# Kernel optimization log

Measured on AMD Instinct MI355X. Metric: run time of the kernel, lower is better.

## Reference

```python
import jax, jax.numpy as jnp
import numpy as np

B, QLEN, KLEN = 4, 512, 1024
KDIM = QDIM = ADIM = 512
H_MA, H_CA = 4, 2
CHUNK = 4
EPS = 1e-6
SHARP = 1.0
SCALE = float(np.sqrt(ADIM))


def moving_sum(x, back, forward):
    # moving sum over last axis with window [i-back, i+forward] (matches F.conv1d with ones filter)
    nb = [(0, 0)] * (x.ndim - 1)
    cs = jnp.cumsum(jnp.pad(x, nb + [(back, forward)]), axis=-1)
    cs = jnp.pad(cs, nb + [(1, 0)])
    w = back + forward + 1
    return cs[..., w:] - cs[..., :-w]


def setup_inputs() -> dict:
    key = jax.random.key(0)
    ks = jax.random.split(key, 16)
    s = 0.02
    f32 = jnp.float32
    return {
        'key_t': jax.random.normal(ks[0], (B, KLEN, KDIM), f32),
        'query': jax.random.normal(ks[1], (B, QLEN, QDIM), f32),
        # monotonic energy params
        'wk_ma': jax.random.normal(ks[2], (KDIM, ADIM), f32) * s,
        'bk_ma': jnp.zeros((ADIM,), f32),
        'wq_ma': jax.random.normal(ks[3], (QDIM, ADIM), f32) * s,
        'bq_ma': jnp.zeros((ADIM,), f32),
        'r': jnp.array([-4.0], f32),
        # chunk energy params
        'wk_ca': jax.random.normal(ks[4], (KDIM, ADIM), f32) * s,
        'bk_ca': jnp.zeros((ADIM,), f32),
        'wq_ca': jax.random.normal(ks[5], (QDIM, ADIM), f32) * s,
        'bq_ca': jnp.zeros((ADIM,), f32),
        # value / output projections
        'wv': jax.random.normal(ks[6], (KDIM, ADIM), f32) * s,
        'bv': jnp.zeros((ADIM,), f32),
        'wo': jax.random.normal(ks[7], (ADIM, ADIM), f32) * s,
        'bo': jnp.zeros((ADIM,), f32),
    }


def reference(key_t, query, wk_ma, bk_ma, wq_ma, bq_ma, r,
              wk_ca, bk_ca, wq_ca, bq_ca, wv, bv, wo, bo):
    # ---- monotonic energy (scaled_dot) -> [B, H_ma, qlen, klen]
    dk = ADIM // H_MA
    k_ma = (key_t @ wk_ma + bk_ma).reshape(B, KLEN, H_MA, dk).transpose(0, 2, 1, 3)
    q_ma = (query @ wq_ma + bq_ma).reshape(B, QLEN, H_MA, dk).transpose(0, 2, 1, 3)
    e_ma = jnp.einsum('bhqd,bhkd->bhqk', q_ma, k_ma) / SCALE + r[0]

    # ---- selection probabilities + safe cumprod of (1 - p) (exclusive, in log space)
    p = jax.nn.sigmoid(e_ma)                              # [B,H,q,k]
    log1mp = jnp.log(jnp.clip(1.0 - p, EPS, 1.0))
    cp = jnp.exp(jnp.cumsum(log1mp, axis=-1) - log1mp)    # exclusive cumprod

    # ---- monotonic alignment alpha via recurrence over query steps (parallel MoChA)
    aw0 = jnp.zeros((B, H_MA, KLEN), p.dtype).at[:, :, 0].set(1.0)

    def step(aw_prev, pc):
        p_i, cp_i = pc  # [B,H,k]
        a = p_i * cp_i * jnp.cumsum(aw_prev / jnp.clip(cp_i, EPS, 1.0), axis=-1)
        return a, a

    _, alpha_q = jax.lax.scan(step, aw0, (jnp.moveaxis(p, 2, 0), jnp.moveaxis(cp, 2, 0)))
    alpha = jnp.moveaxis(alpha_q, 0, 2)                   # [B,H_ma,q,k]

    # ---- chunk energy (scaled_dot, shared across MA heads) -> [B, H_ca, qlen, klen]
    dkc = ADIM // H_CA
    k_ca = (key_t @ wk_ca + bk_ca).reshape(B, KLEN, H_CA, dkc).transpose(0, 2, 1, 3)
    q_ca = (query @ wq_ca + bq_ca).reshape(B, QLEN, H_CA, dkc).transpose(0, 2, 1, 3)
    e_ca = jnp.einsum('bhqd,bhkd->bhqk', q_ca, k_ca) / SCALE

    # ---- efficient chunkwise attention: clipped-exp softmax within moving window
    u = e_ca - jnp.max(e_ca, axis=-1, keepdims=True)
    se = jnp.maximum(jnp.exp(u), 1e-5)                    # [B,H_ca,q,k]
    denom = moving_sum(se, CHUNK - 1, 0)                  # [B,H_ca,q,k]
    frac = alpha[:, :, None] * SHARP / denom[:, None]     # [B,H_ma,H_ca,q,k]
    beta = se[:, None] * moving_sum(frac, 0, CHUNK - 1)   # [B,H_ma,H_ca,q,k]
    beta = beta.reshape(B, H_MA * H_CA, QLEN, KLEN)

    # ---- context vector and output projection
    h = H_MA * H_CA
    dv = ADIM // h
    v = (key_t @ wv + bv).reshape(B, KLEN, h, dv).transpose(0, 2, 1, 3)
    cv = jnp.einsum('bhqk,bhkd->bhqd', beta, v)
    cv = cv.transpose(0, 2, 1, 3).reshape(B, QLEN, ADIM)
    return cv @ wo + bo
```

## Files before the change

### kernel.cpp

```cpp
#include <hip/hip_runtime.h>
#include <hip/hip_bf16.h>
#include <math.h>

#define DEV_INLINE __device__ __forceinline__

typedef float f32x4 __attribute__((ext_vector_type(4)));
typedef short bf16x8 __attribute__((ext_vector_type(8)));
typedef short s16x4 __attribute__((ext_vector_type(4)));

constexpr int B_    = 4;
constexpr int QLEN  = 512;
constexpr int KLEN  = 1024;
constexpr int DIM   = 512;
constexpr int H_MA  = 4;
constexpr int H_CA  = 2;
constexpr int CHUNK = 4;
constexpr float EPS = 1e-6f;
constexpr float INV_SCALE = 1.0f / 22.62741699796952f;


DEV_INLINE unsigned short f2bf(float x) {
    unsigned int u = __float_as_uint(x);
    unsigned int r = u + 0x7FFFu + ((u >> 16) & 1u);
    return (unsigned short)(r >> 16);
}

DEV_INLINE void split2(float x, short& h, short& l) {
    const unsigned short hb = f2bf(x);
    const float hf = __uint_as_float(((unsigned int)hb) << 16);
    h = (short)hb;
    l = (short)f2bf(x - hf);
}

DEV_INLINE float bf2f(short s) {
    return __uint_as_float(((unsigned int)(unsigned short)s) << 16);
}

__global__ __launch_bounds__(256) void rowsplit2_kernel(
    const float* __restrict__ X0, short* __restrict__ H0, short* __restrict__ L0, int n0_4,
    const float* __restrict__ X1, short* __restrict__ H1, short* __restrict__ L1, int n1_4)
{
    int i = blockIdx.x * 256 + threadIdx.x;
    const float* X; short* Xh; short* Xl;
    if (i < n0_4) { X = X0; Xh = H0; Xl = L0; }
    else {
        i -= n0_4;
        if (i >= n1_4) return;
        X = X1; Xh = H1; Xl = L1;
    }
    const f32x4 v = *(const f32x4*)(X + (size_t)i * 4);
    s16x4 h, l;
#pragma unroll
    for (int j = 0; j < 4; ++j) {
        short hh, ll;
        split2(v[j], hh, ll);
        h[j] = hh; l[j] = ll;
    }
    *(s16x4*)(Xh + (size_t)i * 4) = h;
    *(s16x4*)(Xl + (size_t)i * 4) = l;
}

__global__ __launch_bounds__(256) void transsplit6_kernel(
    const float* __restrict__ w0, const float* __restrict__ w1,
    const float* __restrict__ w2, const float* __restrict__ w3,
    const float* __restrict__ w4, const float* __restrict__ w5,
    short* __restrict__ WTkh, short* __restrict__ WTkl,
    short* __restrict__ WTqh, short* __restrict__ WTql,
    short* __restrict__ WToh, short* __restrict__ WTol)
{
    const float* W; short* Dh; short* Dl;
    const int zz = blockIdx.z;
    const int MS = 512 * 512;
    switch (zz) {
        case 0: W = w0; Dh = WTkh;          Dl = WTkl;          break;
        case 1: W = w1; Dh = WTkh + MS;     Dl = WTkl + MS;     break;
        case 2: W = w2; Dh = WTkh + 2 * MS; Dl = WTkl + 2 * MS; break;
        case 3: W = w3; Dh = WTqh;          Dl = WTql;          break;
        case 4: W = w4; Dh = WTqh + MS;     Dl = WTql + MS;     break;
        default: W = w5; Dh = WToh;         Dl = WTol;          break;
    }

    __shared__ __align__(16) short Th[64][72];
    __shared__ __align__(16) short Tl[64][72];
    const int t = threadIdx.x;
    const int k0 = blockIdx.x * 64;
    const int n0 = blockIdx.y * 64;
#pragma unroll
    for (int i = 0; i < 4; ++i) {
        const int c  = t + 256 * i;
        const int kr = c >> 4;
        const int nc = c & 15;
        const f32x4 v = *(const f32x4*)(W + (size_t)(k0 + kr) * DIM + n0 + nc * 4);
#pragma unroll
        for (int j = 0; j < 4; ++j) {
            short h, l;
            split2(v[j], h, l);
            Th[nc * 4 + j][kr] = h;
            Tl[nc * 4 + j][kr] = l;
        }
    }
    __syncthreads();
#pragma unroll
    for (int i = 0; i < 4; ++i) {
        const int c  = t + 256 * i;
        const int nr = c >> 4;
        const int kc = c & 15;
        *(s16x4*)(Dh + (size_t)(n0 + nr) * DIM + k0 + kc * 4) = *(const s16x4*)&Th[nr][kc * 4];
        *(s16x4*)(Dl + (size_t)(n0 + nr) * DIM + k0 + kc * 4) = *(const s16x4*)&Tl[nr][kc * 4];
    }
}


DEV_INLINE void mfma128_nt_core(
    const short* __restrict__ Ah, const short* __restrict__ Al, int lda,
    const short* __restrict__ Bh, const short* __restrict__ Bl, int ldb,
    int K, int bm, int bn, f32x4 (&acc)[4][4])
{
    __shared__ __align__(16) short AsH[8][4][16][8];
    __shared__ __align__(16) short AsL[8][4][16][8];
    __shared__ __align__(16) short BsH[8][4][16][8];
    __shared__ __align__(16) short BsL[8][4][16][8];
    const int tid  = threadIdx.x;
    const int lane = tid & 63;
    const int w    = tid >> 6;
    const int wm   = w >> 1, wn = w & 1;
    const int lkg  = lane >> 4, lrow = lane & 15;

    for (int k0 = 0; k0 < K; k0 += 32) {
        bf16x8 vah[2], val[2], vbh[2], vbl[2];
#pragma unroll
        for (int p = 0; p < 2; ++p) {
            const int c = p * 256 + tid;
            const int row = c >> 2, kk = c & 3;
            const size_t ao = (size_t)(bm + row) * lda + k0 + kk * 8;
            const size_t bo = (size_t)(bn + row) * ldb + k0 + kk * 8;
            vah[p] = *(const bf16x8*)(Ah + ao);
            val[p] = *(const bf16x8*)(Al + ao);
            vbh[p] = *(const bf16x8*)(Bh + bo);
            vbl[p] = *(const bf16x8*)(Bl + bo);
        }
        __syncthreads();
#pragma unroll
        for (int p = 0; p < 2; ++p) {
            const int c = p * 256 + tid;
            const int row = c >> 2, kk = c & 3;
            const int fm = row >> 4, rr = row & 15;
            *(bf16x8*)&AsH[fm][kk][rr][0] = vah[p];
            *(bf16x8*)&AsL[fm][kk][rr][0] = val[p];
            *(bf16x8*)&BsH[fm][kk][rr][0] = vbh[p];
            *(bf16x8*)&BsL[fm][kk][rr][0] = vbl[p];
        }
        __syncthreads();

        bf16x8 bhf[4], blf[4];
#pragma unroll
        for (int fn = 0; fn < 4; ++fn) {
            bhf[fn] = *(const bf16x8*)&BsH[wn * 4 + fn][lkg][lrow][0];
            blf[fn] = *(const bf16x8*)&BsL[wn * 4 + fn][lkg][lrow][0];
        }
#pragma unroll
        for (int fm = 0; fm < 4; ++fm) {
            const bf16x8 ah = *(const bf16x8*)&AsH[wm * 4 + fm][lkg][lrow][0];
            const bf16x8 al = *(const bf16x8*)&AsL[wm * 4 + fm][lkg][lrow][0];
#pragma unroll
            for (int fn = 0; fn < 4; ++fn) {
                acc[fm][fn] = __builtin_amdgcn_mfma_f32_16x16x32_bf16(ah, bhf[fn], acc[fm][fn], 0, 0, 0);
                acc[fm][fn] = __builtin_amdgcn_mfma_f32_16x16x32_bf16(ah, blf[fn], acc[fm][fn], 0, 0, 0);
                acc[fm][fn] = __builtin_amdgcn_mfma_f32_16x16x32_bf16(al, bhf[fn], acc[fm][fn], 0, 0, 0);
            }
        }
    }
}

__global__ __launch_bounds__(256) void proj_both_kernel(
    const short* __restrict__ Kh, const short* __restrict__ Kl,
    const short* __restrict__ Qh, const short* __restrict__ Ql,
    const short* __restrict__ WTkh, const short* __restrict__ WTkl,
    const short* __restrict__ WTqh, const short* __restrict__ WTql,
    short* __restrict__ KPh, short* __restrict__ KPl,
    short* __restrict__ QPh, short* __restrict__ QPl,
    const float* __restrict__ bkma, const float* __restrict__ bkca,
    const float* __restrict__ bvv_,
    const float* __restrict__ bqma, const float* __restrict__ bqca)
{
    const int bid = blockIdx.x;
    const short *Ah, *Al, *Bh, *Bl;
    short *Ch, *Cl;
    const float *b0, *b1, *b2;
    int bm, bn, ldc;
    if (bid < 384) {
        bm = (bid & 31) * 128; bn = (bid >> 5) * 128;
        Ah = Kh; Al = Kl; Bh = WTkh; Bl = WTkl;
        Ch = KPh; Cl = KPl; ldc = 1536;
        b0 = bkma; b1 = bkca; b2 = bvv_;
    } else {
        const int r = bid - 384;
        bm = (r & 15) * 128; bn = (r >> 4) * 128;
        Ah = Qh; Al = Ql; Bh = WTqh; Bl = WTql;
        Ch = QPh; Cl = QPl; ldc = 1024;
        b0 = bqma; b1 = bqca; b2 = bqca;
    }

    f32x4 acc[4][4] = {};
    mfma128_nt_core(Ah, Al, DIM, Bh, Bl, DIM, DIM, bm, bn, acc);
    const int lane = threadIdx.x & 63;
    const int w = threadIdx.x >> 6;
    const int wm = w >> 1, wn = w & 1;
#pragma unroll
    for (int fm = 0; fm < 4; ++fm)
#pragma unroll
        for (int fn = 0; fn < 4; ++fn) {
            const int col = bn + wn * 64 + fn * 16 + (lane & 15);
            const int seg = col >> 9, cs = col & 511;
            const float bvv = seg == 0 ? b0[cs] : (seg == 1 ? b1[cs] : b2[cs]);
#pragma unroll
            for (int j = 0; j < 4; ++j) {
                const int row = bm + wm * 64 + fm * 16 + (lane >> 4) * 4 + j;
                short h, l;
                split2(acc[fm][fn][j] + bvv, h, l);
                Ch[(size_t)row * ldc + col] = h;
                Cl[(size_t)row * ldc + col] = l;
            }
        }
}

__global__ __launch_bounds__(256) void energy_both_kernel(
    const short* __restrict__ QPh, const short* __restrict__ QPl,
    const short* __restrict__ KPh, const short* __restrict__ KPl,
    float* __restrict__ EMA, float* __restrict__ ECA,
    const float* __restrict__ radd)
{
    const int gz = blockIdx.z;
    int colA0, colB0, HD;
    float* E;
    float addv;
    int b, h;
    if (gz < 16) {
        b = gz >> 2; h = gz & 3;
        colA0 = 0; colB0 = 0; HD = 128;
        E = EMA + (size_t)gz * QLEN * KLEN;
        addv = radd[0];
    } else {
        const int z = gz - 16;
        b = z >> 1; h = z & 1;
        colA0 = 512; colB0 = 512; HD = 256;
        E = ECA + (size_t)z * QLEN * KLEN;
        addv = 0.0f;
    }
    const short* Ah = QPh + (size_t)b * QLEN * 1024 + colA0 + h * HD;
    const short* Al = QPl + (size_t)b * QLEN * 1024 + colA0 + h * HD;
    const short* Bh = KPh + (size_t)b * KLEN * 1536 + colB0 + h * HD;
    const short* Bl = KPl + (size_t)b * KLEN * 1536 + colB0 + h * HD;

    f32x4 acc[4][4] = {};
    const int bm = blockIdx.x * 128, bn = blockIdx.y * 128;
    mfma128_nt_core(Ah, Al, 1024, Bh, Bl, 1536, HD, bm, bn, acc);
    const int lane = threadIdx.x & 63;
    const int w = threadIdx.x >> 6;
    const int wm = w >> 1, wn = w & 1;
#pragma unroll
    for (int fm = 0; fm < 4; ++fm)
#pragma unroll
        for (int fn = 0; fn < 4; ++fn) {
            const int col = bn + wn * 64 + fn * 16 + (lane & 15);
#pragma unroll
            for (int j = 0; j < 4; ++j) {
                const int row = bm + wm * 64 + fm * 16 + (lane >> 4) * 4 + j;
                E[(size_t)row * KLEN + col] = acc[fm][fn][j] * INV_SCALE + addv;
            }
        }
}


DEV_INLINE void mfma_nt_core(const short* __restrict__ Ah, const short* __restrict__ Al, int lda,
                             const short* __restrict__ Bh, const short* __restrict__ Bl, int ldb,
                             int K, int bm, int bn, f32x4 (&acc)[2][2])
{
    __shared__ __align__(16) short AsH[4][4][16][8];
    __shared__ __align__(16) short AsL[4][4][16][8];
    __shared__ __align__(16) short BsH[4][4][16][8];
    __shared__ __align__(16) short BsL[4][4][16][8];
    const int tid  = threadIdx.x;
    const int lane = tid & 63;
    const int w    = tid >> 6;
    const int wm   = w >> 1, wn = w & 1;
    const int r    = tid >> 2;
    const int kg   = tid & 3;
    const int rb   = r >> 4, rr = r & 15;
    const int lkg  = lane >> 4, lrr = lane & 15;

    for (int k0 = 0; k0 < K; k0 += 32) {
        const bf16x8 avh = *(const bf16x8*)(Ah + (size_t)(bm + r) * lda + k0 + kg * 8);
        const bf16x8 avl = *(const bf16x8*)(Al + (size_t)(bm + r) * lda + k0 + kg * 8);
        const bf16x8 bvh = *(const bf16x8*)(Bh + (size_t)(bn + r) * ldb + k0 + kg * 8);
        const bf16x8 bvl = *(const bf16x8*)(Bl + (size_t)(bn + r) * ldb + k0 + kg * 8);
        __syncthreads();
        *(bf16x8*)&AsH[rb][kg][rr][0] = avh;
        *(bf16x8*)&AsL[rb][kg][rr][0] = avl;
        *(bf16x8*)&BsH[rb][kg][rr][0] = bvh;
        *(bf16x8*)&BsL[rb][kg][rr][0] = bvl;
        __syncthreads();
#pragma unroll
        for (int fm = 0; fm < 2; ++fm) {
            const bf16x8 ah = *(const bf16x8*)&AsH[wm * 2 + fm][lkg][lrr][0];
            const bf16x8 al = *(const bf16x8*)&AsL[wm * 2 + fm][lkg][lrr][0];
#pragma unroll
            for (int fn = 0; fn < 2; ++fn) {
                const bf16x8 bh = *(const bf16x8*)&BsH[wn * 2 + fn][lkg][lrr][0];
                const bf16x8 bl = *(const bf16x8*)&BsL[wn * 2 + fn][lkg][lrr][0];
                acc[fm][fn] = __builtin_amdgcn_mfma_f32_16x16x32_bf16(ah, bh, acc[fm][fn], 0, 0, 0);
                acc[fm][fn] = __builtin_amdgcn_mfma_f32_16x16x32_bf16(ah, bl, acc[fm][fn], 0, 0, 0);
                acc[fm][fn] = __builtin_amdgcn_mfma_f32_16x16x32_bf16(al, bh, acc[fm][fn], 0, 0, 0);
            }
        }
    }
}

__global__ __launch_bounds__(256) void mfma_nt_f32_kernel(
    const short* __restrict__ Ah, const short* __restrict__ Al, int lda,
    const short* __restrict__ Bh, const short* __restrict__ Bl, int ldb,
    float* __restrict__ C, int ldc, int K,
    const float* __restrict__ bias)
{
    f32x4 acc[2][2] = {};
    const int bm = blockIdx.x * 64, bn = blockIdx.y * 64;
    mfma_nt_core(Ah, Al, lda, Bh, Bl, ldb, K, bm, bn, acc);
    const int lane = threadIdx.x & 63;
    const int w = threadIdx.x >> 6;
    const int wm = w >> 1, wn = w & 1;
#pragma unroll
    for (int fm = 0; fm < 2; ++fm)
#pragma unroll
        for (int fn = 0; fn < 2; ++fn) {
            const int col = bn + wn * 32 + fn * 16 + (lane & 15);
            const float bvv = bias ? bias[col] : 0.0f;
#pragma unroll
            for (int j = 0; j < 4; ++j) {
                const int row = bm + wm * 32 + fm * 16 + (lane >> 4) * 4 + j;
                C[(size_t)row * ldc + col] = acc[fm][fn][j] + bvv;
            }
        }
}


__global__ __launch_bounds__(256) void rows_kernel(
    float* __restrict__ PCP, float* __restrict__ ICP,
    float* __restrict__ SE, float* __restrict__ RDEN)
{
    const int bid = blockIdx.x;
    const int tid = threadIdx.x;
    const int lane = tid & 63, wid = tid >> 6;

    if (bid < B_ * H_MA * QLEN) {
        const size_t row = bid;
        float* pe = PCP + row * KLEN;
        float* pi = ICP + row * KLEN;

        const float4 ev = *(const float4*)(pe + tid * 4);
        float e[4] = {ev.x, ev.y, ev.z, ev.w};
        float p[4], l[4], s[4];
        float run = 0.0f;
#pragma unroll
        for (int j = 0; j < 4; ++j) {
            p[j] = 1.0f / (1.0f + expf(-e[j]));
            float om = 1.0f - p[j];
            om = fminf(fmaxf(om, EPS), 1.0f);
            l[j] = logf(om);
            run += l[j];
            s[j] = run;
        }
        const float t = run;
        float v = t;
#pragma unroll
        for (int off = 1; off < 64; off <<= 1) {
            const float u = __shfl_up(v, off);
            if (lane >= off) v += u;
        }
        __shared__ float wsum[4];
        if (lane == 63) wsum[wid] = v;
        __syncthreads();
        float base = v - t;
        for (int w = 0; w < wid; ++w) base += wsum[w];

        float4 po, io;
        float* pp = (float*)&po;
        float* ip = (float*)&io;
#pragma unroll
        for (int j = 0; j < 4; ++j) {
            const float cum = base + s[j];
            const float cp  = expf(cum - l[j]);
            pp[j] = p[j] * cp;
            ip[j] = 1.0f / fmaxf(cp, EPS);
        }
        *(float4*)(pe + tid * 4) = po;
        *(float4*)(pi + tid * 4) = io;
    } else {
        const size_t row = bid - B_ * H_MA * QLEN;
        float* ps = SE + row * KLEN;
        float* pd = RDEN + row * KLEN;

        const float4 ev = *(const float4*)(ps + tid * 4);
        float e[4] = {ev.x, ev.y, ev.z, ev.w};
        float m = fmaxf(fmaxf(e[0], e[1]), fmaxf(e[2], e[3]));
#pragma unroll
        for (int off = 32; off >= 1; off >>= 1)
            m = fmaxf(m, __shfl_xor(m, off));
        __shared__ float wmax[4];
        if (lane == 0) wmax[wid] = m;
        __syncthreads();
        m = fmaxf(fmaxf(wmax[0], wmax[1]), fmaxf(wmax[2], wmax[3]));

        __shared__ float sh[KLEN + 3];
        if (tid < 3) sh[tid] = 0.0f;
        float se[4];
#pragma unroll
        for (int j = 0; j < 4; ++j) {
            se[j] = fmaxf(expf(e[j] - m), 1e-5f);
            sh[3 + tid * 4 + j] = se[j];
        }
        __syncthreads();
        float4 so, do_;
        float* sp = (float*)&so;
        float* dp = (float*)&do_;
#pragma unroll
        for (int j = 0; j < 4; ++j) {
            const int k = tid * 4 + j;
            sp[j] = se[j];
            dp[j] = 1.0f / (sh[3 + k] + sh[2 + k] + sh[1 + k] + sh[k]);
        }
        *(float4*)(ps + tid * 4) = so;
        *(float4*)(pd + tid * 4) = do_;
    }
}


template<int CTRL, int ROW_MASK>
DEV_INLINE float dpp_add(float x) {
    int t = __builtin_amdgcn_update_dpp(0, __float_as_int(x), CTRL, ROW_MASK, 0xf, true);
    return x + __int_as_float(t);
}

DEV_INLINE float wave64_incl_scan(float x) {
    x = dpp_add<0x111, 0xf>(x);
    x = dpp_add<0x112, 0xf>(x);
    x = dpp_add<0x114, 0xf>(x);
    x = dpp_add<0x118, 0xf>(x);
    x = dpp_add<0x142, 0xa>(x);
    x = dpp_add<0x143, 0xc>(x);
    return x;
}

typedef __attribute__((address_space(3))) void lv_t;
typedef __attribute__((address_space(1))) const void gv_t;

DEV_INLINE void dma16(const float* g, float* l) {
    __builtin_amdgcn_global_load_lds((gv_t*)g, (lv_t*)l, 16, 0, 0);
}

template<int N> DEV_INLINE void vwait() {
    asm volatile("s_waitcnt vmcnt(%0)" :: "i"(N) : "memory");
    __builtin_amdgcn_sched_barrier(0);
}

template<int N> DEV_INLINE void lwait() {
    asm volatile("s_waitcnt lgkmcnt(%0)" :: "i"(N));
    __builtin_amdgcn_sched_barrier(0);
}

DEV_INLINE void ldsr4(f32x4& d, const float* a_) {
    const unsigned off = (unsigned)(size_t)(lv_t*)a_;
    asm volatile("ds_read_b128 %0, %1" : "=v"(d) : "v"(off));
}

DEV_INLINE void dswr1(float* a_, float v) {
    const unsigned off = (unsigned)(size_t)(lv_t*)a_;
    asm volatile("ds_write_b32 %0, %1" :: "v"(off), "v"(v));
}

DEV_INLINE void sbar() {
    asm volatile("s_barrier" ::: "memory");
}

#define ASTEP(WAITN, BUF, NBUF, PAR, DO_READ, DO_DMA, CG, NG)         \
    {                                                                 \
        vwait<WAITN>();                                               \
        if (DO_READ) {                                                \
            ldsr4(p##NG, &ring[NBUF][0][qoff]);                       \
            ldsr4(i##NG, &ring[NBUF][1][qoff]);                       \
        }                                                             \
        const float t0 = a0 * i##CG[0];                               \
        const float t1 = a1 * i##CG[1];                               \
        const float t2 = a2 * i##CG[2];                               \
        const float t3 = a3 * i##CG[3];                               \
        const float s1 = t0 + t1;                                     \
        const float s2 = s1 + t2;                                     \
        const float s3 = s2 + t3;                                     \
        const float incl = wave64_incl_scan(s3);                      \
        const float excl = incl - s3;                                 \
        if (lane == 63) dswr1(&tot[PAR][wq], incl);                   \
        lwait<0>();                                                   \
        sbar();                                                       \
        f32x4 T;                                                      \
        ldsr4(T, &tot[PAR][0]);                                       \
        lwait<0>();                                                   \
        float Tpre = excl;                                            \
        if (wq > 0) Tpre += T[0];                                     \
        if (wq > 1) Tpre += T[1];                                     \
        if (wq > 2) Tpre += T[2];                                     \
        a0 = p##CG[0] * (Tpre + t0);                                  \
        a1 = p##CG[1] * (Tpre + s1);                                  \
        a2 = p##CG[2] * (Tpre + s2);                                  \
        a3 = p##CG[3] * (Tpre + s3);                                  \
        f32x4 av = {a0, a1, a2, a3};                                  \
        *(f32x4*)st = av;                                             \
        st += KLEN;                                                   \
        __builtin_amdgcn_sched_barrier(0);                            \
        if (DO_DMA) {                                                 \
            dma16(np, &ring[BUF][0][wq * 256]);                       \
            dma16(ni, &ring[BUF][1][wq * 256]);                       \
            np += KLEN; ni += KLEN;                                   \
        }                                                             \
    }

__global__ __launch_bounds__(256) void alpha_kernel(
    const float* __restrict__ PCPin, const float* __restrict__ ICP,
    float* __restrict__ AOUT)
{
    __shared__ __align__(16) float ring[8][2][1024];
    __shared__ __align__(16) float tot[2][4];

    const int z = blockIdx.x;
    const float* base = PCPin + (size_t)z * QLEN * KLEN;
    const float* ibase = ICP + (size_t)z * QLEN * KLEN;
    float* obase = AOUT + (size_t)z * QLEN * KLEN;
    const int tid  = threadIdx.x;
    const int lane = tid & 63;
    const int wq   = tid >> 6;
    const int qoff = wq * 256 + lane * 4;

    {
        const float* pp = base + qoff;
        const float* ip = ibase + qoff;
#pragma unroll
        for (int rr = 0; rr < 8; ++rr) {
            dma16(pp, &ring[rr][0][wq * 256]);
            dma16(ip, &ring[rr][1][wq * 256]);
            pp += KLEN; ip += KLEN;
        }
    }

    f32x4 pA, iA, pB, iB;
    vwait<14>();
    ldsr4(pA, &ring[0][0][qoff]);
    ldsr4(iA, &ring[0][1][qoff]);
    lwait<0>();

    float a0 = 0.0f, a1 = 0.0f, a2 = 0.0f, a3 = 0.0f;
    if (qoff == 0) a0 = 1.0f;

    float* st = obase + qoff;
    const float* np = base + (size_t)8 * KLEN + qoff;
    const float* ni = ibase + (size_t)8 * KLEN + qoff;

    for (int it = 0; it < 63; ++it) {
        ASTEP(12, 0, 1, 0, true, true, A, B)
        ASTEP(12, 1, 2, 1, true, true, B, A)
        ASTEP(12, 2, 3, 0, true, true, A, B)
        ASTEP(12, 3, 4, 1, true, true, B, A)
        ASTEP(12, 4, 5, 0, true, true, A, B)
        ASTEP(12, 5, 6, 1, true, true, B, A)
        ASTEP(12, 6, 7, 0, true, true, A, B)
        ASTEP(12, 7, 0, 1, true, true, B, A)
    }

    ASTEP(12, 0, 1, 0, true, false, A, B)
    ASTEP(10, 1, 2, 1, true, false, B, A)
    ASTEP(8,  2, 3, 0, true, false, A, B)
    ASTEP(6,  3, 4, 1, true, false, B, A)
    ASTEP(4,  4, 5, 0, true, false, A, B)
    ASTEP(2,  5, 6, 1, true, false, B, A)
    ASTEP(0,  6, 7, 0, true, false, A, B)
    ASTEP(0,  7, 0, 1, false, false, B, A)
}


__global__ __launch_bounds__(256) void fused_cv_kernel(
    const float* __restrict__ ALPHA, const float* __restrict__ SE,
    const float* __restrict__ RDEN,
    const short* __restrict__ VPh, const short* __restrict__ VPl, int ldv,
    short* __restrict__ CVh, short* __restrict__ CVl)
{
    const int z = blockIdx.y;
    const int b = z >> 3;
    const int h = z & 7;
    const int hma = h >> 1;
    const int hca = h & 1;
    const int bm = blockIdx.x * 64;

    const float* a_base  = ALPHA + ((size_t)b * H_MA + hma) * QLEN * KLEN;
    const float* se_base = SE   + ((size_t)b * H_CA + hca) * QLEN * KLEN;
    const float* dn_base = RDEN + ((size_t)b * H_CA + hca) * QLEN * KLEN;
    const short* vh_base = VPh + (size_t)b * KLEN * ldv + 1024 + h * 64;
    const short* vl_base = VPl + (size_t)b * KLEN * ldv + 1024 + h * 64;
    short* Ch = CVh + (size_t)b * QLEN * DIM + h * 64;
    short* Cl = CVl + (size_t)b * QLEN * DIM + h * 64;

    __shared__ float As[16][68];
    __shared__ float Bs[16][68];
    const int tid  = threadIdx.x;
    const int tm   = (tid >> 4) << 2;
    const int tn   = (tid & 15) << 2;
    const int arow = tid >> 2;
    const int acol = (tid & 3) << 2;
    const int brow = tid >> 4;
    const int bcol = (tid & 15) << 2;
    float acc[4][4] = {};

    for (int k0 = 0; k0 < KLEN; k0 += 16) {
        const int ka = k0 + acol;
        const size_t roff = (size_t)(bm + arow) * KLEN;
        const f32x4 sev = *(const f32x4*)(se_base + roff + ka);
        const f32x4 al0 = *(const f32x4*)(a_base + roff + ka);
        const f32x4 dn0 = *(const f32x4*)(dn_base + roff + ka);
        f32x4 al1 = {0.0f, 0.0f, 0.0f, 0.0f};
        f32x4 dn1 = {1.0f, 1.0f, 1.0f, 1.0f};
        if (ka + 4 < KLEN) {
            al1 = *(const f32x4*)(a_base + roff + ka + 4);
            dn1 = *(const f32x4*)(dn_base + roff + ka + 4);
        }
        float ad[7];
#pragma unroll
        for (int j = 0; j < 4; ++j) ad[j] = al0[j] * dn0[j];
#pragma unroll
        for (int j = 0; j < 3; ++j) ad[4 + j] = al1[j] * dn1[j];
        const s16x4 vh4 = *(const s16x4*)(vh_base + (size_t)(k0 + brow) * ldv + bcol);
        const s16x4 vl4 = *(const s16x4*)(vl_base + (size_t)(k0 + brow) * ldv + bcol);
        __syncthreads();
        As[acol + 0][arow] = sev[0] * (ad[0] + ad[1] + ad[2] + ad[3]);
        As[acol + 1][arow] = sev[1] * (ad[1] + ad[2] + ad[3] + ad[4]);
        As[acol + 2][arow] = sev[2] * (ad[2] + ad[3] + ad[4] + ad[5]);
        As[acol + 3][arow] = sev[3] * (ad[3] + ad[4] + ad[5] + ad[6]);
#pragma unroll
        for (int j = 0; j < 4; ++j)
            Bs[brow][bcol + j] = bf2f(vh4[j]) + bf2f(vl4[j]);
        __syncthreads();
#pragma unroll
        for (int kk = 0; kk < 16; ++kk) {
            const float4 av = *(const float4*)&As[kk][tm];
            const float4 bw = *(const float4*)&Bs[kk][tn];
            const float ar[4] = {av.x, av.y, av.z, av.w};
            const float br[4] = {bw.x, bw.y, bw.z, bw.w};
#pragma unroll
            for (int i = 0; i < 4; ++i)
#pragma unroll
                for (int j = 0; j < 4; ++j)
                    acc[i][j] = fmaf(ar[i], br[j], acc[i][j]);
        }
    }
#pragma unroll
    for (int i = 0; i < 4; ++i) {
        s16x4 oh, ol;
#pragma unroll
        for (int j = 0; j < 4; ++j) {
            short hh, ll;
            split2(acc[i][j], hh, ll);
            oh[j] = hh; ol[j] = ll;
        }
        const size_t ro = (size_t)(bm + tm + i) * DIM + tn;
        *(s16x4*)(Ch + ro) = oh;
        *(s16x4*)(Cl + ro) = ol;
    }
}


extern "C" void kernel_launch(void* const* d_in, const int* in_sizes, int n_in,
                              void* d_out, int out_size, void* d_ws, size_t ws_size,
                              hipStream_t stream)
{
    (void)in_sizes; (void)n_in; (void)out_size; (void)ws_size;
    const float* key_t = (const float*)d_in[0];
    const float* query = (const float*)d_in[1];
    const float* wk_ma = (const float*)d_in[2];
    const float* bk_ma = (const float*)d_in[3];
    const float* wq_ma = (const float*)d_in[4];
    const float* bq_ma = (const float*)d_in[5];
    const float* r     = (const float*)d_in[6];
    const float* wk_ca = (const float*)d_in[7];
    const float* bk_ca = (const float*)d_in[8];
    const float* wq_ca = (const float*)d_in[9];
    const float* bq_ca = (const float*)d_in[10];
    const float* wv    = (const float*)d_in[11];
    const float* bv    = (const float*)d_in[12];
    const float* wo    = (const float*)d_in[13];
    const float* bo    = (const float*)d_in[14];
    float* out = (float*)d_out;

    char* w8 = (char*)d_ws;
    size_t off = 0;
    auto take = [&](size_t n) { char* p = w8 + off; off += n; return p; };
    float* PCP = (float*)take(32ull << 20);
    float* ICP = (float*)take(32ull << 20);
    float* SE  = (float*)take(16ull << 20);
    float* DEN = (float*)take(16ull << 20);
    char* keyrg = take(8ull << 20);
    short* keyh = (short*)keyrg;
    short* keyl = (short*)(keyrg + (4ull << 20));
    short* CVh  = (short*)keyrg;
    short* CVl  = (short*)(keyrg + (2ull << 20));
    short* qh = (short*)take(2ull << 20);
    short* ql = (short*)take(2ull << 20);
    short* WTkh = (short*)take((size_t)1536 * 512 * 2);
    short* WTkl = (short*)take((size_t)1536 * 512 * 2);
    short* WTqh = (short*)take((size_t)1024 * 512 * 2);
    short* WTql = (short*)take((size_t)1024 * 512 * 2);
    short* WToh = (short*)take((size_t)512 * 512 * 2);
    short* WTol = (short*)take((size_t)512 * 512 * 2);
    short* KPh = (short*)take((size_t)4096 * 1536 * 2);
    short* KPl = (short*)take((size_t)4096 * 1536 * 2);
    short* QPh = (short*)take((size_t)2048 * 1024 * 2);
    short* QPl = (short*)take((size_t)2048 * 1024 * 2);

    const dim3 blk(256);
    const int KEL4 = B_ * KLEN * DIM / 4;
    const int QEL4 = B_ * QLEN * DIM / 4;

    rowsplit2_kernel<<<dim3((KEL4 + QEL4 + 255) / 256), blk, 0, stream>>>(
        key_t, keyh, keyl, KEL4, query, qh, ql, QEL4);
    transsplit6_kernel<<<dim3(8, 8, 6), blk, 0, stream>>>(
        wk_ma, wk_ca, wv, wq_ma, wq_ca, wo,
        WTkh, WTkl, WTqh, WTql, WToh, WTol);

    proj_both_kernel<<<dim3(512), blk, 0, stream>>>(
        keyh, keyl, qh, ql, WTkh, WTkl, WTqh, WTql,
        KPh, KPl, QPh, QPl, bk_ma, bk_ca, bv, bq_ma, bq_ca);

    energy_both_kernel<<<dim3(QLEN / 128, KLEN / 128, 24), blk, 0, stream>>>(
        QPh, QPl, KPh, KPl, PCP, SE, r);

    rows_kernel<<<dim3(B_ * H_MA * QLEN + B_ * H_CA * QLEN), blk, 0, stream>>>(
        PCP, ICP, SE, DEN);

    alpha_kernel<<<dim3(B_ * H_MA), blk, 0, stream>>>(PCP, ICP, PCP);

    fused_cv_kernel<<<dim3(QLEN / 64, B_ * H_MA * H_CA), blk, 0, stream>>>(
        PCP, SE, DEN, KPh, KPl, 1536, CVh, CVl);

    mfma_nt_f32_kernel<<<dim3(B_ * QLEN / 64, DIM / 64), blk, 0, stream>>>(
        CVh, CVl, DIM, WToh, WTol, DIM, out, DIM, DIM, bo);
}
```

Before: 328.6 us.

## Compute context vectors with split-bf16 MFMA instead of FP32 FMA loop

```diff
diff --git a/kernel.cpp b/kernel.cpp
--- a/kernel.cpp
+++ b/kernel.cpp
@@ -584,7 +584,7 @@
 }
 
 
-__global__ __launch_bounds__(256) void fused_cv_kernel(
+__global__ __launch_bounds__(256) void fused_cv_mfma_kernel(
     const float* __restrict__ ALPHA, const float* __restrict__ SE,
     const float* __restrict__ RDEN,
     const short* __restrict__ VPh, const short* __restrict__ VPl, int ldv,
@@ -605,71 +605,96 @@
     short* Ch = CVh + (size_t)b * QLEN * DIM + h * 64;
     short* Cl = CVl + (size_t)b * QLEN * DIM + h * 64;
 
-    __shared__ float As[16][68];
-    __shared__ float Bs[16][68];
+    __shared__ __align__(16) short AsH[4][4][16][8];
+    __shared__ __align__(16) short AsL[4][4][16][8];
+    __shared__ __align__(16) short BsH[4][4][16][8];
+    __shared__ __align__(16) short BsL[4][4][16][8];
+
     const int tid  = threadIdx.x;
-    const int tm   = (tid >> 4) << 2;
-    const int tn   = (tid & 15) << 2;
+    const int lane = tid & 63;
+    const int w    = tid >> 6;
+    const int wm   = w >> 1, wn = w & 1;
+    const int lkg  = lane >> 4, lrr = lane & 15;
     const int arow = tid >> 2;
-    const int acol = (tid & 3) << 2;
-    const int brow = tid >> 4;
-    const int bcol = (tid & 15) << 2;
-    float acc[4][4] = {};
-
-    for (int k0 = 0; k0 < KLEN; k0 += 16) {
-        const int ka = k0 + acol;
+    const int aoct = tid & 3;
+    const int vk  = tid >> 3;
+    const int vn8 = (tid & 7) * 8;
+
+    f32x4 acc[2][2] = {};
+
+    for (int k0 = 0; k0 < KLEN; k0 += 32) {
+        const int ka = k0 + aoct * 8;
         const size_t roff = (size_t)(bm + arow) * KLEN;
-        const f32x4 sev = *(const f32x4*)(se_base + roff + ka);
+        const f32x4 se0 = *(const f32x4*)(se_base + roff + ka);
+        const f32x4 se1 = *(const f32x4*)(se_base + roff + ka + 4);
         const f32x4 al0 = *(const f32x4*)(a_base + roff + ka);
+        const f32x4 al1 = *(const f32x4*)(a_base + roff + ka + 4);
         const f32x4 dn0 = *(const f32x4*)(dn_base + roff + ka);
-        f32x4 al1 = {0.0f, 0.0f, 0.0f, 0.0f};
-        f32x4 dn1 = {1.0f, 1.0f, 1.0f, 1.0f};
-        if (ka + 4 < KLEN) {
-            al1 = *(const f32x4*)(a_base + roff + ka + 4);
-            dn1 = *(const f32x4*)(dn_base + roff + ka + 4);
-        }
-        float ad[7];
+        const f32x4 dn1 = *(const f32x4*)(dn_base + roff + ka + 4);
+        f32x4 al2 = {0.0f, 0.0f, 0.0f, 0.0f};
+        f32x4 dn2 = {1.0f, 1.0f, 1.0f, 1.0f};
+        if (ka + 8 < KLEN) {
+            al2 = *(const f32x4*)(a_base + roff + ka + 8);
+            dn2 = *(const f32x4*)(dn_base + roff + ka + 8);
+        }
+        float ad[11];
 #pragma unroll
         for (int j = 0; j < 4; ++j) ad[j] = al0[j] * dn0[j];
 #pragma unroll
-        for (int j = 0; j < 3; ++j) ad[4 + j] = al1[j] * dn1[j];
-        const s16x4 vh4 = *(const s16x4*)(vh_base + (size_t)(k0 + brow) * ldv + bcol);
-        const s16x4 vl4 = *(const s16x4*)(vl_base + (size_t)(k0 + brow) * ldv + bcol);
-        __syncthreads();
-        As[acol + 0][arow] = sev[0] * (ad[0] + ad[1] + ad[2] + ad[3]);
-        As[acol + 1][arow] = sev[1] * (ad[1] + ad[2] + ad[3] + ad[4]);
-        As[acol + 2][arow] = sev[2] * (ad[2] + ad[3] + ad[4] + ad[5]);
-        As[acol + 3][arow] = sev[3] * (ad[3] + ad[4] + ad[5] + ad[6]);
-#pragma unroll
-        for (int j = 0; j < 4; ++j)
-            Bs[brow][bcol + j] = bf2f(vh4[j]) + bf2f(vl4[j]);
-        __syncthreads();
-#pragma unroll
-        for (int kk = 0; kk < 16; ++kk) {
-            const float4 av = *(const float4*)&As[kk][tm];
-            const float4 bw = *(const float4*)&Bs[kk][tn];
-            const float ar[4] = {av.x, av.y, av.z, av.w};
-            const float br[4] = {bw.x, bw.y, bw.z, bw.w};
-#pragma unroll
-            for (int i = 0; i < 4; ++i)
-#pragma unroll
-                for (int j = 0; j < 4; ++j)
-                    acc[i][j] = fmaf(ar[i], br[j], acc[i][j]);
-        }
-    }
-#pragma unroll
-    for (int i = 0; i < 4; ++i) {
-        s16x4 oh, ol;
-#pragma unroll
-        for (int j = 0; j < 4; ++j) {
+        for (int j = 0; j < 4; ++j) ad[4 + j] = al1[j] * dn1[j];
+#pragma unroll
+        for (int j = 0; j < 3; ++j) ad[8 + j] = al2[j] * dn2[j];
+        bf16x8 bh_, bl_;
+#pragma unroll
+        for (int j = 0; j < 8; ++j) {
+            const float sej = j < 4 ? se0[j] : se1[j - 4];
+            const float beta = sej * (ad[j] + ad[j + 1] + ad[j + 2] + ad[j + 3]);
             short hh, ll;
-            split2(acc[i][j], hh, ll);
-            oh[j] = hh; ol[j] = ll;
-        }
-        const size_t ro = (size_t)(bm + tm + i) * DIM + tn;
-        *(s16x4*)(Ch + ro) = oh;
-        *(s16x4*)(Cl + ro) = ol;
-    }
+            split2(beta, hh, ll);
+            bh_[j] = hh; bl_[j] = ll;
+        }
+        const bf16x8 vvh = *(const bf16x8*)(vh_base + (size_t)(k0 + vk) * ldv + vn8);
+        const bf16x8 vvl = *(const bf16x8*)(vl_base + (size_t)(k0 + vk) * ldv + vn8);
+        __syncthreads();
+        *(bf16x8*)&AsH[arow >> 4][aoct][arow & 15][0] = bh_;
+        *(bf16x8*)&AsL[arow >> 4][aoct][arow & 15][0] = bl_;
+#pragma unroll
+        for (int j = 0; j < 8; ++j) {
+            const int n = vn8 + j;
+            BsH[n >> 4][vk >> 3][n & 15][vk & 7] = vvh[j];
+            BsL[n >> 4][vk >> 3][n & 15][vk & 7] = vvl[j];
+        }
+        __syncthreads();
+#pragma unroll
+        for (int fm = 0; fm < 2; ++fm) {
+            const bf16x8 ah = *(const bf16x8*)&AsH[wm * 2 + fm][lkg][lrr][0];
+            const bf16x8 al = *(const bf16x8*)&AsL[wm * 2 + fm][lkg][lrr][0];
+#pragma unroll
+            for (int fn = 0; fn < 2; ++fn) {
+                const bf16x8 vh = *(const bf16x8*)&BsH[wn * 2 + fn][lkg][lrr][0];
+                const bf16x8 vl = *(const bf16x8*)&BsL[wn * 2 + fn][lkg][lrr][0];
+                acc[fm][fn] = __builtin_amdgcn_mfma_f32_16x16x32_bf16(ah, vh, acc[fm][fn], 0, 0, 0);
+                acc[fm][fn] = __builtin_amdgcn_mfma_f32_16x16x32_bf16(ah, vl, acc[fm][fn], 0, 0, 0);
+                acc[fm][fn] = __builtin_amdgcn_mfma_f32_16x16x32_bf16(al, vh, acc[fm][fn], 0, 0, 0);
+            }
+        }
+    }
+
+#pragma unroll
+    for (int fm = 0; fm < 2; ++fm)
+#pragma unroll
+        for (int fn = 0; fn < 2; ++fn) {
+            const int col = wn * 32 + fn * 16 + (lane & 15);
+#pragma unroll
+            for (int j = 0; j < 4; ++j) {
+                const int row = bm + wm * 32 + fm * 16 + (lane >> 4) * 4 + j;
+                short hh, ll;
+                split2(acc[fm][fn][j], hh, ll);
+                const size_t ro = (size_t)row * DIM + col;
+                Ch[ro] = hh;
+                Cl[ro] = ll;
+            }
+        }
 }
 
 
@@ -742,7 +767,7 @@
 
     alpha_kernel<<<dim3(B_ * H_MA), blk, 0, stream>>>(PCP, ICP, PCP);
 
-    fused_cv_kernel<<<dim3(QLEN / 64, B_ * H_MA * H_CA), blk, 0, stream>>>(
+    fused_cv_mfma_kernel<<<dim3(QLEN / 64, B_ * H_MA * H_CA), blk, 0, stream>>>(
         PCP, SE, DEN, KPh, KPl, 1536, CVh, CVl);
 
     mfma_nt_f32_kernel<<<dim3(B_ * QLEN / 64, DIM / 64), blk, 0, stream>>>(
```

Result: faster. 296.7 us (median of 2 runs) (-9.7%).
